# Kernel optimization log

Hardware: AMD Instinct MI355X
Metric: run time of the kernel (lower is better)

The kernel has to match this reference:

```python
import jax, jax.numpy as jnp
import numpy as np
import math

B, S, D, H = 2, 2048, 1024, 16
HD = D // H  # head_dim = 64


def setup_inputs() -> dict:
    rng = jax.random.key(0)
    ks = jax.random.split(rng, 11)
    std = 1.0 / math.sqrt(D)
    inp = {
        "query": jax.random.normal(ks[0], (B, S, D), dtype=jnp.float32),
        "key": jax.random.normal(ks[1], (B, S, D), dtype=jnp.float32),
        "value": jax.random.normal(ks[2], (B, S, D), dtype=jnp.float32),
        # causal mask: True = masked (ignored), matching masked_fill semantics
        "mask": jnp.triu(jnp.ones((S, S), dtype=bool), k=1),
        "wq": jax.random.normal(ks[3], (D, D), dtype=jnp.float32) * std,
        "bq": jnp.zeros((D,), dtype=jnp.float32),
        "wk": jax.random.normal(ks[4], (D, D), dtype=jnp.float32) * std,
        "bk": jnp.zeros((D,), dtype=jnp.float32),
        "wv": jax.random.normal(ks[5], (D, D), dtype=jnp.float32) * std,
        "bv": jnp.zeros((D,), dtype=jnp.float32),
        "wo": jax.random.normal(ks[6], (D, D), dtype=jnp.float32) * std,
        "bo": jnp.zeros((D,), dtype=jnp.float32),
    }
    return inp


def reference(query, key, value, mask, wq, bq, wk, bk, wv, bv, wo, bo):
    # Linear projections (torch Linear: x @ W.T + b)
    q = jnp.einsum('bsd,ed->bse', query, wq) + bq
    k = jnp.einsum('bsd,ed->bse', key, wk) + bk
    v = jnp.einsum('bsd,ed->bse', value, wv) + bv
    # split heads: (B, S, D) -> (B, H, S, HD)
    q = q.reshape(B, S, H, HD).transpose(0, 2, 1, 3)
    k = k.reshape(B, S, H, HD).transpose(0, 2, 1, 3)
    v = v.reshape(B, S, H, HD).transpose(0, 2, 1, 3)
    # naive attention: materialize full (B, H, Sq, Sk) scores
    scores = jnp.einsum('bhqd,bhkd->bhqk', q, k) / jnp.sqrt(jnp.float32(HD))
    scores = jnp.where(mask[None, None, :, :], -jnp.inf, scores)
    attn = jax.nn.softmax(scores, axis=-1)
    out = jnp.einsum('bhqk,bhkd->bhqd', attn, v)
    out = out.transpose(0, 2, 1, 3).reshape(B, S, D)
    return jnp.einsum('bsd,ed->bse', out, wo) + bo
```

## Files before the change

kernel.cpp:

```cpp
#include <hip/hip_runtime.h>
#include <stdint.h>

#define B_ 2
#define S_ 2048
#define D_ 1024
#define H_ 16
#define HD_ 64
#define M_TOT (B_*S_)

typedef __bf16 bf16;
typedef bf16 bf16x8 __attribute__((ext_vector_type(8)));
typedef float f32x4 __attribute__((ext_vector_type(4)));
typedef float f32x16 __attribute__((ext_vector_type(16)));
typedef unsigned int u32;
typedef unsigned int u32x4v __attribute__((ext_vector_type(4)));

__device__ __forceinline__ void gload_lds16(const void* g, void* l) {
    __builtin_amdgcn_global_load_lds((const __attribute__((address_space(1))) void*)g,
                                     (__attribute__((address_space(3))) void*)l, 16, 0, 0);
}

__device__ __forceinline__ u32 cvtpk_bf16(float lo, float hi) {
    u32 d;
    asm("v_cvt_pk_bf16_f32 %0, %1, %2" : "=v"(d) : "v"(lo), "v"(hi));
    return d;
}

__global__ __launch_bounds__(256) void cvt_kernel(
    const float* __restrict__ q, const float* __restrict__ k, const float* __restrict__ v,
    const float* __restrict__ wq, const float* __restrict__ wk,
    const float* __restrict__ wv, const float* __restrict__ wo,
    bf16* __restrict__ xq, bf16* __restrict__ xk, bf16* __restrict__ xv,
    bf16* __restrict__ wqb, bf16* __restrict__ wkb, bf16* __restrict__ wvb, bf16* __restrict__ wob)
{
    const float* src; bf16* dst; int n;
    switch (blockIdx.y) {
        case 0: src=q;  dst=xq;  n=M_TOT*D_; break;
        case 1: src=k;  dst=xk;  n=M_TOT*D_; break;
        case 2: src=v;  dst=xv;  n=M_TOT*D_; break;
        case 3: src=wq; dst=wqb; n=D_*D_;    break;
        case 4: src=wk; dst=wkb; n=D_*D_;    break;
        case 5: src=wv; dst=wvb; n=D_*D_;    break;
        default: src=wo; dst=wob; n=D_*D_;   break;
    }
    int i = (blockIdx.x*blockDim.x + threadIdx.x)*8;
    if (i >= n) return;
    const f32x4* s4 = (const f32x4*)(src + i);
    f32x4 a = s4[0], b = s4[1];
    bf16x8 o;
    #pragma unroll
    for (int j = 0; j < 4; ++j) { o[j] = (bf16)a[j]; o[j+4] = (bf16)b[j]; }
    *(bf16x8*)(dst + i) = o;
}

__device__ __forceinline__ void gemm_mainloop(const bf16* __restrict__ A, const bf16* __restrict__ Wt,
                                              int brow, int bcol, bf16* As, bf16* Bs,
                                              f32x4 (&acc)[4][4])
{
    const int tid = threadIdx.x;
    const int l = tid & 63, w = tid >> 6;
    const int wr = w >> 1, wc = w & 1;
    const int lr = l & 15, lq = l >> 4;

    for (int k0 = 0; k0 < D_; k0 += 32) {
        #pragma unroll
        for (int i = 0; i < 2; ++i) {
            int id = i*256 + tid;
            int row = id >> 2, c8 = (id & 3) << 3;
            gload_lds16(A  + (size_t)(brow + row)*D_ + k0 + c8, As + id*8);
            gload_lds16(Wt + (size_t)(bcol + row)*D_ + k0 + c8, Bs + id*8);
        }
        __syncthreads();
        bf16x8 af[4], bf[4];
        #pragma unroll
        for (int m = 0; m < 4; ++m)
            af[m] = *(const bf16x8*)&As[(wr*64 + m*16 + lr)*32 + lq*8];
        #pragma unroll
        for (int n = 0; n < 4; ++n)
            bf[n] = *(const bf16x8*)&Bs[(wc*64 + n*16 + lr)*32 + lq*8];
        #pragma unroll
        for (int m = 0; m < 4; ++m)
            #pragma unroll
            for (int n = 0; n < 4; ++n)
                acc[m][n] = __builtin_amdgcn_mfma_f32_16x16x32_bf16(af[m], bf[n], acc[m][n], 0, 0, 0);
        __syncthreads();
    }
}

__global__ __launch_bounds__(256) void gemm_qkv(
    const bf16* __restrict__ xq, const bf16* __restrict__ xk, const bf16* __restrict__ xv,
    const bf16* __restrict__ wqb, const bf16* __restrict__ wkb, const bf16* __restrict__ wvb,
    const float* __restrict__ bq, const float* __restrict__ bk, const float* __restrict__ bv,
    bf16* __restrict__ Qf, bf16* __restrict__ Kf, bf16* __restrict__ Vf)
{
    __shared__ __align__(16) bf16 As[128*32];
    __shared__ __align__(16) bf16 Bs[128*32];
    const int z = blockIdx.z;
    const bf16* A  = (z==0) ? xq  : (z==1) ? xk  : xv;
    const bf16* Wt = (z==0) ? wqb : (z==1) ? wkb : wvb;
    const float* bias = (z==0) ? bq : (z==1) ? bk : bv;

    const int brow = (blockIdx.x & 31)*128;
    const int bcol = (blockIdx.x >> 5)*128;

    f32x4 acc[4][4] = {};
    gemm_mainloop(A, Wt, brow, bcol, As, Bs, acc);

    const int tid = threadIdx.x;
    const int l = tid & 63, w = tid >> 6;
    const int wr = w >> 1, wc = w & 1;
    const int lr = l & 15, lq = l >> 4;

    #pragma unroll
    for (int m = 0; m < 4; ++m)
        #pragma unroll
        for (int n = 0; n < 4; ++n) {
            int col = bcol + wc*64 + n*16 + lr;
            float bv_ = bias[col];
            int h = col >> 6, hd = col & 63;
            #pragma unroll
            for (int r = 0; r < 4; ++r) {
                int row = brow + wr*64 + m*16 + lq*4 + r;
                int b = row >> 11, s = row & 2047;
                float val = acc[m][n][r] + bv_;
                if (z == 0) val *= 0.18033688011112042f;
                size_t hbase = ((size_t)b*H_ + h)*S_*HD_;
                if (z < 2) {
                    int chunk = ((s >> 5) << 2) + (hd >> 4);
                    int lane  = (((hd >> 3) & 1) << 5) | (s & 31);
                    bf16* dst = (z==0) ? Qf : Kf;
                    dst[hbase + (size_t)chunk*512 + lane*8 + (hd & 7)] = (bf16)val;
                } else {
                    int chunk = ((s >> 6) << 3) + (((s >> 4) & 3) << 1) + (hd >> 5);
                    int lane  = (((s >> 3) & 1) << 5) | (hd & 31);
                    Vf[hbase + (size_t)chunk*512 + lane*8 + (s & 7)] = (bf16)val;
                }
            }
        }
}

__global__ __launch_bounds__(256) void gemm_out(
    const bf16* __restrict__ Oat, const bf16* __restrict__ wob,
    const float* __restrict__ bo, float* __restrict__ out)
{
    __shared__ __align__(16) bf16 As[128*32];
    __shared__ __align__(16) bf16 Bs[128*32];
    const int brow = (blockIdx.x & 31)*128;
    const int bcol = (blockIdx.x >> 5)*128;

    f32x4 acc[4][4] = {};
    gemm_mainloop(Oat, wob, brow, bcol, As, Bs, acc);

    const int tid = threadIdx.x;
    const int l = tid & 63, w = tid >> 6;
    const int wr = w >> 1, wc = w & 1;
    const int lr = l & 15, lq = l >> 4;

    #pragma unroll
    for (int m = 0; m < 4; ++m)
        #pragma unroll
        for (int n = 0; n < 4; ++n) {
            int col = bcol + wc*64 + n*16 + lr;
            float bv_ = bo[col];
            #pragma unroll
            for (int r = 0; r < 4; ++r) {
                int row = brow + wr*64 + m*16 + lq*4 + r;
                out[(size_t)row*D_ + col] = acc[m][n][r] + bv_;
            }
        }
}

#define ATTN_BODY(CUR, NXT, KT) do {                                                        \
    const int kc0_ = (KT)*64;                                                               \
    const bool last_ = ((KT) == nkt - 1);                                                   \
    const int ktn_ = ((KT) + 1 < nkt) ? (KT) + 1 : (KT);                                    \
    _Pragma("unroll")                                                                       \
    for (int kv2 = 0; kv2 < 2; ++kv2)                                                       \
        _Pragma("unroll")                                                                   \
        for (int dc = 0; dc < 4; ++dc)                                                      \
            NXT[kv2][dc] = *(const bf16x8*)(Kfp + (size_t)((ktn_*2 + kv2)*4 + dc)*512 + l8);\
    bf16x8 va0[4], va1[4];                                                                  \
    _Pragma("unroll")                                                                       \
    for (int c = 0; c < 4; ++c) {                                                           \
        va0[c] = *(const bf16x8*)(Vfp + (size_t)((KT)*8 + c*2 + 0)*512 + l8);               \
        va1[c] = *(const bf16x8*)(Vfp + (size_t)((KT)*8 + c*2 + 1)*512 + l8);               \
    }                                                                                       \
    f32x16 ct0 = {}, ct1 = {};                                                              \
    _Pragma("unroll")                                                                       \
    for (int dc = 0; dc < 4; ++dc)                                                          \
        ct0 = __builtin_amdgcn_mfma_f32_32x32x16_bf16(CUR[0][dc], qb[dc], ct0, 0, 0, 0);    \
    _Pragma("unroll")                                                                       \
    for (int dc = 0; dc < 4; ++dc)                                                          \
        ct1 = __builtin_amdgcn_mfma_f32_32x32x16_bf16(CUR[1][dc], qb[dc], ct1, 0, 0, 0);    \
    if (last_) {                                                                            \
        _Pragma("unroll")                                                                   \
        for (int reg = 0; reg < 16; ++reg) {                                                \
            const int rr = (reg & 3) + 8*(reg >> 2) + 4*hi;                                 \
            if (kc0_ + rr > qrow)      ct0[reg] = -1e30f;                                   \
            if (kc0_ + 32 + rr > qrow) ct1[reg] = -1e30f;                                   \
        }                                                                                   \
    }                                                                                       \
    float t8[8];                                                                            \
    _Pragma("unroll")                                                                       \
    for (int i = 0; i < 8; ++i)                                                             \
        t8[i] = fmaxf(fmaxf(ct0[i], ct0[i+8]), fmaxf(ct1[i], ct1[i+8]));                    \
    float t4a = fmaxf(t8[0], t8[4]), t4b = fmaxf(t8[1], t8[5]);                             \
    float t4c = fmaxf(t8[2], t8[6]), t4d = fmaxf(t8[3], t8[7]);                             \
    float vm = fmaxf(fmaxf(t4a, t4b), fmaxf(t4c, t4d));                                     \
    vm = fmaxf(vm, __shfl_xor(vm, 32));                                                     \
    if (!__all(vm <= mrun + 8.f)) {                                                         \
        float nm = fmaxf(mrun, vm);                                                         \
        float al = exp2f(mrun - nm);                                                        \
        _Pragma("unroll")                                                                   \
        for (int i = 0; i < 16; ++i) { ot0[i] *= al; ot1[i] *= al; }                        \
        lrun *= al;                                                                         \
        mrun = nm;                                                                          \
    }                                                                                       \
    _Pragma("unroll")                                                                       \
    for (int i = 0; i < 16; ++i) {                                                          \
        ct0[i] = exp2f(ct0[i] - mrun);                                                      \
        ct1[i] = exp2f(ct1[i] - mrun);                                                      \
    }                                                                                       \
    float s8[8];                                                                            \
    _Pragma("unroll")                                                                       \
    for (int i = 0; i < 8; ++i)                                                             \
        s8[i] = (ct0[i] + ct0[i+8]) + (ct1[i] + ct1[i+8]);                                  \
    float s4a = s8[0]+s8[4], s4b = s8[1]+s8[5], s4c = s8[2]+s8[6], s4d = s8[3]+s8[7];       \
    float ps = (s4a + s4b) + (s4c + s4d);                                                   \
    ps += __shfl_xor(ps, 32);                                                               \
    lrun += ps;                                                                             \
    u32 own0[8], own1[8], oth0[8], oth1[8];                                                 \
    _Pragma("unroll")                                                                       \
    for (int u = 0; u < 8; ++u) {                                                           \
        own0[u] = cvtpk_bf16(ct0[2*u], ct0[2*u+1]);                                         \
        own1[u] = cvtpk_bf16(ct1[2*u], ct1[2*u+1]);                                         \
    }                                                                                       \
    _Pragma("unroll")                                                                       \
    for (int u = 0; u < 8; ++u) {                                                           \
        oth0[u] = __shfl_xor(own0[u], 32);                                                  \
        oth1[u] = __shfl_xor(own1[u], 32);                                                  \
    }                                                                                       \
    _Pragma("unroll")                                                                       \
    for (int c = 0; c < 4; ++c) {                                                           \
        const int b0 = 4*(c & 1);                                                           \
        u32 o0, o1, o2, o3, x0, x1, x2, x3;                                                 \
        if ((c >> 1) == 0) {                                                                \
            o0 = own0[b0]; o1 = own0[b0+1]; o2 = own0[b0+2]; o3 = own0[b0+3];               \
            x0 = oth0[b0]; x1 = oth0[b0+1]; x2 = oth0[b0+2]; x3 = oth0[b0+3];               \
        } else {                                                                            \
            o0 = own1[b0]; o1 = own1[b0+1]; o2 = own1[b0+2]; o3 = own1[b0+3];               \
            x0 = oth1[b0]; x1 = oth1[b0+1]; x2 = oth1[b0+2]; x3 = oth1[b0+3];               \
        }                                                                                   \
        u32 w0 = hi ? x2 : o0;                                                              \
        u32 w1 = hi ? x3 : o1;                                                              \
        u32 w2 = hi ? o2 : x0;                                                              \
        u32 w3 = hi ? o3 : x1;                                                              \
        u32x4v pw = { w0, w1, w2, w3 };                                                     \
        bf16x8 pb = __builtin_bit_cast(bf16x8, pw);                                         \
        ot0 = __builtin_amdgcn_mfma_f32_32x32x16_bf16(va0[c], pb, ot0, 0, 0, 0);            \
        ot1 = __builtin_amdgcn_mfma_f32_32x32x16_bf16(va1[c], pb, ot1, 0, 0, 0);            \
    }                                                                                       \
} while (0)

__global__ __launch_bounds__(64, 2) void attn_kernel(
    const bf16* __restrict__ Qf, const bf16* __restrict__ Kf,
    const bf16* __restrict__ Vf, bf16* __restrict__ Oat)
{
    __shared__ __align__(16) char Osm[32*128];

    const int l = threadIdx.x & 63;
    const int l31 = l & 31, hi = l >> 5;

    const int id = (int)blockIdx.x;
    const int xcd = id & 7, slot = id >> 3;
    const int bh  = xcd + 8*(slot >> 6);
    const int s6 = slot & 63;
    const int sb = s6 & 31;
    const int g  = ((sb & 7) << 3) | (sb >> 3);
    const int qt = (s6 < 32) ? g : 63 - g;
    const int b = bh >> 4, h = bh & 15;
    const int q0 = qt*32;
    const int qrow = q0 + l31;

    const bf16* Qfp = Qf + (size_t)bh*S_*HD_;
    const bf16* Kfp = Kf + (size_t)bh*S_*HD_;
    const bf16* Vfp = Vf + (size_t)bh*S_*HD_;
    const int l8 = l*8;

    bf16x8 qb[4];
    #pragma unroll
    for (int dc = 0; dc < 4; ++dc)
        qb[dc] = *(const bf16x8*)(Qfp + (size_t)(((q0 >> 5) << 2) + dc)*512 + l8);

    f32x16 ot0 = {}, ot1 = {};
    float mrun = -1e30f, lrun = 0.f;
    const int nkt = q0/64 + 1;

    bf16x8 ka[2][4], kb[2][4];
    #pragma unroll
    for (int kv2 = 0; kv2 < 2; ++kv2)
        #pragma unroll
        for (int dc = 0; dc < 4; ++dc)
            ka[kv2][dc] = *(const bf16x8*)(Kfp + (size_t)(kv2*4 + dc)*512 + l8);

    int kt = 0;
    while (kt + 1 < nkt) {
        ATTN_BODY(ka, kb, kt); ++kt;
        ATTN_BODY(kb, ka, kt); ++kt;
    }
    if (kt < nkt) {
        ATTN_BODY(ka, kb, kt);
    }

    const float inv = 1.f / lrun;
    #pragma unroll
    for (int rp = 0; rp < 16; rp += 2) {
        const int d0 = (rp & 3) + 8*(rp >> 2) + 4*hi;
        u32 p0 = cvtpk_bf16(ot0[rp]*inv, ot0[rp+1]*inv);
        u32 p1 = cvtpk_bf16(ot1[rp]*inv, ot1[rp+1]*inv);
        const int swz = (l31 & 7) << 4;
        *(u32*)(Osm + l31*128 + (( d0*2)        ^ swz)) = p0;
        *(u32*)(Osm + l31*128 + (((32 + d0)*2)  ^ swz)) = p1;
    }
    #pragma unroll
    for (int p = 0; p < 4; ++p) {
        const int row  = p*8 + (l >> 3);
        const int colb = (l & 7)*16;
        u32x4v v = *(const u32x4v*)(Osm + row*128 + (colb ^ ((row & 7) << 4)));
        char* gp = (char*)Oat + (((size_t)(b*S_ + q0 + row)*D_ + h*64)*2) + colb;
        *(u32x4v*)gp = v;
    }
}

extern "C" void kernel_launch(void* const* d_in, const int* in_sizes, int n_in,
                              void* d_out, int out_size, void* d_ws, size_t ws_size,
                              hipStream_t stream) {
    const float* q  = (const float*)d_in[0];
    const float* k  = (const float*)d_in[1];
    const float* v  = (const float*)d_in[2];
    const float* wq = (const float*)d_in[4];
    const float* bq = (const float*)d_in[5];
    const float* wk = (const float*)d_in[6];
    const float* bk = (const float*)d_in[7];
    const float* wv = (const float*)d_in[8];
    const float* bv = (const float*)d_in[9];
    const float* wo = (const float*)d_in[10];
    const float* bo = (const float*)d_in[11];
    float* out = (float*)d_out;

    char* p = (char*)d_ws;
    const size_t XSZ = (size_t)M_TOT*D_*sizeof(bf16);
    const size_t WSZ = (size_t)D_*D_*sizeof(bf16);
    bf16* xq  = (bf16*)p; p += XSZ;
    bf16* xk  = (bf16*)p; p += XSZ;
    bf16* xv  = (bf16*)p; p += XSZ;
    bf16* wqb = (bf16*)p; p += WSZ;
    bf16* wkb = (bf16*)p; p += WSZ;
    bf16* wvb = (bf16*)p; p += WSZ;
    bf16* wob = (bf16*)p; p += WSZ;
    bf16* Qf  = (bf16*)p; p += XSZ;
    bf16* Kf  = (bf16*)p; p += XSZ;
    bf16* Vf  = (bf16*)p; p += XSZ;
    bf16* Oat = (bf16*)p; p += XSZ;

    cvt_kernel<<<dim3(2048, 7), 256, 0, stream>>>(q, k, v, wq, wk, wv, wo,
                                                  xq, xk, xv, wqb, wkb, wvb, wob);
    gemm_qkv<<<dim3(256, 1, 3), 256, 0, stream>>>(xq, xk, xv, wqb, wkb, wvb,
                                                  bq, bk, bv, Qf, Kf, Vf);
    attn_kernel<<<2048, 64, 0, stream>>>(Qf, Kf, Vf, Oat);
    gemm_out<<<dim3(256), 256, 0, stream>>>(Oat, wob, bo, out);
}
```

Baseline: 139.6 us.

## Software-pipeline attention: compute next tile's QK scores during current softmax

```diff
diff --git a/kernel.cpp b/kernel.cpp
--- a/kernel.cpp
+++ b/kernel.cpp
@@ -170,40 +170,46 @@
         }
 }
 
-#define ATTN_BODY(CUR, NXT, KT) do {                                                        \
-    const int kc0_ = (KT)*64;                                                               \
-    const bool last_ = ((KT) == nkt - 1);                                                   \
-    const int ktn_ = ((KT) + 1 < nkt) ? (KT) + 1 : (KT);                                    \
-    _Pragma("unroll")                                                                       \
-    for (int kv2 = 0; kv2 < 2; ++kv2)                                                       \
+#define PIPE_ITER(CT0, CT1, NT0, NT1, KN, KP, T) do {                                       \
+    const int T_ = (T);                                                                     \
+    const int kc0_ = T_*64;                                                                 \
+    const bool last_ = (T_ == nkt - 1);                                                     \
+    if (T_ + 2 < nkt) {                                                                     \
+        _Pragma("unroll")                                                                   \
+        for (int kv2 = 0; kv2 < 2; ++kv2)                                                   \
+            _Pragma("unroll")                                                               \
+            for (int dc = 0; dc < 4; ++dc)                                                  \
+                KP[kv2][dc] = *(const bf16x8*)(Kfp + (size_t)(((T_+2)*2 + kv2)*4 + dc)*512 + l8); \
+    }                                                                                       \
+    bf16x8 va0[4], va1[4];                                                                  \
+    _Pragma("unroll")                                                                       \
+    for (int c = 0; c < 4; ++c) {                                                           \
+        va0[c] = *(const bf16x8*)(Vfp + (size_t)(T_*8 + c*2 + 0)*512 + l8);                 \
+        va1[c] = *(const bf16x8*)(Vfp + (size_t)(T_*8 + c*2 + 1)*512 + l8);                 \
+    }                                                                                       \
+    if (T_ + 1 < nkt) {                                                                     \
+        NT0 = (f32x16){}; NT1 = (f32x16){};                                                 \
+        __builtin_amdgcn_s_setprio(1);                                                      \
         _Pragma("unroll")                                                                   \
         for (int dc = 0; dc < 4; ++dc)                                                      \
-            NXT[kv2][dc] = *(const bf16x8*)(Kfp + (size_t)((ktn_*2 + kv2)*4 + dc)*512 + l8);\
-    bf16x8 va0[4], va1[4];                                                                  \
-    _Pragma("unroll")                                                                       \
-    for (int c = 0; c < 4; ++c) {                                                           \
-        va0[c] = *(const bf16x8*)(Vfp + (size_t)((KT)*8 + c*2 + 0)*512 + l8);               \
-        va1[c] = *(const bf16x8*)(Vfp + (size_t)((KT)*8 + c*2 + 1)*512 + l8);               \
-    }                                                                                       \
-    f32x16 ct0 = {}, ct1 = {};                                                              \
-    _Pragma("unroll")                                                                       \
-    for (int dc = 0; dc < 4; ++dc)                                                          \
-        ct0 = __builtin_amdgcn_mfma_f32_32x32x16_bf16(CUR[0][dc], qb[dc], ct0, 0, 0, 0);    \
-    _Pragma("unroll")                                                                       \
-    for (int dc = 0; dc < 4; ++dc)                                                          \
-        ct1 = __builtin_amdgcn_mfma_f32_32x32x16_bf16(CUR[1][dc], qb[dc], ct1, 0, 0, 0);    \
+            NT0 = __builtin_amdgcn_mfma_f32_32x32x16_bf16(KN[0][dc], qb[dc], NT0, 0, 0, 0); \
+        _Pragma("unroll")                                                                   \
+        for (int dc = 0; dc < 4; ++dc)                                                      \
+            NT1 = __builtin_amdgcn_mfma_f32_32x32x16_bf16(KN[1][dc], qb[dc], NT1, 0, 0, 0); \
+        __builtin_amdgcn_s_setprio(0);                                                      \
+    }                                                                                       \
     if (last_) {                                                                            \
         _Pragma("unroll")                                                                   \
         for (int reg = 0; reg < 16; ++reg) {                                                \
             const int rr = (reg & 3) + 8*(reg >> 2) + 4*hi;                                 \
-            if (kc0_ + rr > qrow)      ct0[reg] = -1e30f;                                   \
-            if (kc0_ + 32 + rr > qrow) ct1[reg] = -1e30f;                                   \
+            if (kc0_ + rr > qrow)      CT0[reg] = -1e30f;                                   \
+            if (kc0_ + 32 + rr > qrow) CT1[reg] = -1e30f;                                   \
         }                                                                                   \
     }                                                                                       \
     float t8[8];                                                                            \
     _Pragma("unroll")                                                                       \
     for (int i = 0; i < 8; ++i)                                                             \
-        t8[i] = fmaxf(fmaxf(ct0[i], ct0[i+8]), fmaxf(ct1[i], ct1[i+8]));                    \
+        t8[i] = fmaxf(fmaxf(CT0[i], CT0[i+8]), fmaxf(CT1[i], CT1[i+8]));                    \
     float t4a = fmaxf(t8[0], t8[4]), t4b = fmaxf(t8[1], t8[5]);                             \
     float t4c = fmaxf(t8[2], t8[6]), t4d = fmaxf(t8[3], t8[7]);                             \
     float vm = fmaxf(fmaxf(t4a, t4b), fmaxf(t4c, t4d));                                     \
@@ -218,48 +224,58 @@
     }                                                                                       \
     _Pragma("unroll")                                                                       \
     for (int i = 0; i < 16; ++i) {                                                          \
-        ct0[i] = exp2f(ct0[i] - mrun);                                                      \
-        ct1[i] = exp2f(ct1[i] - mrun);                                                      \
+        CT0[i] = exp2f(CT0[i] - mrun);                                                      \
+        CT1[i] = exp2f(CT1[i] - mrun);                                                      \
     }                                                                                       \
     float s8[8];                                                                            \
     _Pragma("unroll")                                                                       \
     for (int i = 0; i < 8; ++i)                                                             \
-        s8[i] = (ct0[i] + ct0[i+8]) + (ct1[i] + ct1[i+8]);                                  \
+        s8[i] = (CT0[i] + CT0[i+8]) + (CT1[i] + CT1[i+8]);                                  \
     float s4a = s8[0]+s8[4], s4b = s8[1]+s8[5], s4c = s8[2]+s8[6], s4d = s8[3]+s8[7];       \
     float ps = (s4a + s4b) + (s4c + s4d);                                                   \
     ps += __shfl_xor(ps, 32);                                                               \
     lrun += ps;                                                                             \
-    u32 own0[8], own1[8], oth0[8], oth1[8];                                                 \
+    u32 own0[8], own1[8];                                                                   \
     _Pragma("unroll")                                                                       \
     for (int u = 0; u < 8; ++u) {                                                           \
-        own0[u] = cvtpk_bf16(ct0[2*u], ct0[2*u+1]);                                         \
-        own1[u] = cvtpk_bf16(ct1[2*u], ct1[2*u+1]);                                         \
-    }                                                                                       \
-    _Pragma("unroll")                                                                       \
-    for (int u = 0; u < 8; ++u) {                                                           \
-        oth0[u] = __shfl_xor(own0[u], 32);                                                  \
-        oth1[u] = __shfl_xor(own1[u], 32);                                                  \
-    }                                                                                       \
+        own0[u] = cvtpk_bf16(CT0[2*u], CT0[2*u+1]);                                         \
+        own1[u] = cvtpk_bf16(CT1[2*u], CT1[2*u+1]);                                         \
+    }                                                                                       \
+                   \
+    u32 rcv0[4], rcv1[4];                                                                   \
+    {                                                                                       \
+        u32 s0_ = hi ? own0[0] : own0[2];  u32 s1_ = hi ? own0[1] : own0[3];                \
+        u32 s2_ = hi ? own0[4] : own0[6];  u32 s3_ = hi ? own0[5] : own0[7];                \
+        rcv0[0] = __shfl_xor(s0_, 32); rcv0[1] = __shfl_xor(s1_, 32);                       \
+        rcv0[2] = __shfl_xor(s2_, 32); rcv0[3] = __shfl_xor(s3_, 32);                       \
+        u32 t0_ = hi ? own1[0] : own1[2];  u32 t1_ = hi ? own1[1] : own1[3];                \
+        u32 t2_ = hi ? own1[4] : own1[6];  u32 t3_ = hi ? own1[5] : own1[7];                \
+        rcv1[0] = __shfl_xor(t0_, 32); rcv1[1] = __shfl_xor(t1_, 32);                       \
+        rcv1[2] = __shfl_xor(t2_, 32); rcv1[3] = __shfl_xor(t3_, 32);                       \
+    }                                                                                       \
+    __builtin_amdgcn_s_setprio(1);                                                          \
     _Pragma("unroll")                                                                       \
     for (int c = 0; c < 4; ++c) {                                                           \
         const int b0 = 4*(c & 1);                                                           \
-        u32 o0, o1, o2, o3, x0, x1, x2, x3;                                                 \
+        const int p0 = b0 >> 1;                                                             \
+        u32 oa, ob, oc, od, ra, rb;                                                         \
         if ((c >> 1) == 0) {                                                                \
-            o0 = own0[b0]; o1 = own0[b0+1]; o2 = own0[b0+2]; o3 = own0[b0+3];               \
-            x0 = oth0[b0]; x1 = oth0[b0+1]; x2 = oth0[b0+2]; x3 = oth0[b0+3];               \
+            oa = own0[b0]; ob = own0[b0+1]; oc = own0[b0+2]; od = own0[b0+3];               \
+            ra = rcv0[p0]; rb = rcv0[p0+1];                                                 \
         } else {                                                                            \
-            o0 = own1[b0]; o1 = own1[b0+1]; o2 = own1[b0+2]; o3 = own1[b0+3];               \
-            x0 = oth1[b0]; x1 = oth1[b0+1]; x2 = oth1[b0+2]; x3 = oth1[b0+3];               \
+            oa = own1[b0]; ob = own1[b0+1]; oc = own1[b0+2]; od = own1[b0+3];               \
+            ra = rcv1[p0]; rb = rcv1[p0+1];                                                 \
         }                                                                                   \
-        u32 w0 = hi ? x2 : o0;                                                              \
-        u32 w1 = hi ? x3 : o1;                                                              \
-        u32 w2 = hi ? o2 : x0;                                                              \
-        u32 w3 = hi ? o3 : x1;                                                              \
+        u32 w0 = hi ? ra : oa;                                                              \
+        u32 w1 = hi ? rb : ob;                                                              \
+        u32 w2 = hi ? oc : ra;                                                              \
+        u32 w3 = hi ? od : rb;                                                              \
         u32x4v pw = { w0, w1, w2, w3 };                                                     \
         bf16x8 pb = __builtin_bit_cast(bf16x8, pw);                                         \
         ot0 = __builtin_amdgcn_mfma_f32_32x32x16_bf16(va0[c], pb, ot0, 0, 0, 0);            \
         ot1 = __builtin_amdgcn_mfma_f32_32x32x16_bf16(va1[c], pb, ot1, 0, 0, 0);            \
     }                                                                                       \
+    __builtin_amdgcn_s_setprio(0);                                                          \
 } while (0)
 
 __global__ __launch_bounds__(64, 2) void attn_kernel(
@@ -270,6 +286,7 @@
 
     const int l = threadIdx.x & 63;
     const int l31 = l & 31, hi = l >> 5;
+    const int l8 = l*8;
 
     const int id = (int)blockIdx.x;
     const int xcd = id & 7, slot = id >> 3;
@@ -285,7 +302,6 @@
     const bf16* Qfp = Qf + (size_t)bh*S_*HD_;
     const bf16* Kfp = Kf + (size_t)bh*S_*HD_;
     const bf16* Vfp = Vf + (size_t)bh*S_*HD_;
-    const int l8 = l*8;
 
     bf16x8 qb[4];
     #pragma unroll
@@ -302,14 +318,26 @@
         #pragma unroll
         for (int dc = 0; dc < 4; ++dc)
             ka[kv2][dc] = *(const bf16x8*)(Kfp + (size_t)(kv2*4 + dc)*512 + l8);
-
-    int kt = 0;
-    while (kt + 1 < nkt) {
-        ATTN_BODY(ka, kb, kt); ++kt;
-        ATTN_BODY(kb, ka, kt); ++kt;
-    }
-    if (kt < nkt) {
-        ATTN_BODY(ka, kb, kt);
+    #pragma unroll
+    for (int kv2 = 0; kv2 < 2; ++kv2)
+        #pragma unroll
+        for (int dc = 0; dc < 4; ++dc)
+            kb[kv2][dc] = *(const bf16x8*)(Kfp + (size_t)((2 + kv2)*4 + dc)*512 + l8);
+
+    f32x16 ctA0 = {}, ctA1 = {}, ctB0 = {}, ctB1 = {};
+    #pragma unroll
+    for (int dc = 0; dc < 4; ++dc)
+        ctA0 = __builtin_amdgcn_mfma_f32_32x32x16_bf16(ka[0][dc], qb[dc], ctA0, 0, 0, 0);
+    #pragma unroll
+    for (int dc = 0; dc < 4; ++dc)
+        ctA1 = __builtin_amdgcn_mfma_f32_32x32x16_bf16(ka[1][dc], qb[dc], ctA1, 0, 0, 0);
+
+    int t = 0;
+    for (;;) {
+        PIPE_ITER(ctA0, ctA1, ctB0, ctB1, kb, ka, t);
+        if (++t >= nkt) break;
+        PIPE_ITER(ctB0, ctB1, ctA0, ctA1, ka, kb, t);
+        if (++t >= nkt) break;
     }
 
     const float inv = 1.f / lrun;
```

Measured after the change: 141.5 us. About the same (+1.3%).

## Split attention KV range across two workgroups and merge with combine kernel

Applied to the files above, without the earlier changes.

```diff
diff --git a/kernel.cpp b/kernel.cpp
--- a/kernel.cpp
+++ b/kernel.cpp
@@ -173,7 +173,7 @@
 #define ATTN_BODY(CUR, NXT, KT) do {                                                        \
     const int kc0_ = (KT)*64;                                                               \
     const bool last_ = ((KT) == nkt - 1);                                                   \
-    const int ktn_ = ((KT) + 1 < nkt) ? (KT) + 1 : (KT);                                    \
+    const int ktn_ = ((KT) + 1 < te) ? (KT) + 1 : (KT);                                     \
     _Pragma("unroll")                                                                       \
     for (int kv2 = 0; kv2 < 2; ++kv2)                                                       \
         _Pragma("unroll")                                                                   \
@@ -186,12 +186,14 @@
         va1[c] = *(const bf16x8*)(Vfp + (size_t)((KT)*8 + c*2 + 1)*512 + l8);               \
     }                                                                                       \
     f32x16 ct0 = {}, ct1 = {};                                                              \
+    __builtin_amdgcn_s_setprio(1);                                                          \
     _Pragma("unroll")                                                                       \
     for (int dc = 0; dc < 4; ++dc)                                                          \
         ct0 = __builtin_amdgcn_mfma_f32_32x32x16_bf16(CUR[0][dc], qb[dc], ct0, 0, 0, 0);    \
     _Pragma("unroll")                                                                       \
     for (int dc = 0; dc < 4; ++dc)                                                          \
         ct1 = __builtin_amdgcn_mfma_f32_32x32x16_bf16(CUR[1][dc], qb[dc], ct1, 0, 0, 0);    \
+    __builtin_amdgcn_s_setprio(0);                                                          \
     if (last_) {                                                                            \
         _Pragma("unroll")                                                                   \
         for (int reg = 0; reg < 16; ++reg) {                                                \
@@ -240,6 +242,7 @@
         oth0[u] = __shfl_xor(own0[u], 32);                                                  \
         oth1[u] = __shfl_xor(own1[u], 32);                                                  \
     }                                                                                       \
+    __builtin_amdgcn_s_setprio(1);                                                          \
     _Pragma("unroll")                                                                       \
     for (int c = 0; c < 4; ++c) {                                                           \
         const int b0 = 4*(c & 1);                                                           \
@@ -260,32 +263,34 @@
         ot0 = __builtin_amdgcn_mfma_f32_32x32x16_bf16(va0[c], pb, ot0, 0, 0, 0);            \
         ot1 = __builtin_amdgcn_mfma_f32_32x32x16_bf16(va1[c], pb, ot1, 0, 0, 0);            \
     }                                                                                       \
+    __builtin_amdgcn_s_setprio(0);                                                          \
 } while (0)
 
-__global__ __launch_bounds__(64, 2) void attn_kernel(
+__global__ __launch_bounds__(64, 4) void attn_part(
     const bf16* __restrict__ Qf, const bf16* __restrict__ Kf,
-    const bf16* __restrict__ Vf, bf16* __restrict__ Oat)
-{
-    __shared__ __align__(16) char Osm[32*128];
-
+    const bf16* __restrict__ Vf, bf16* __restrict__ Opart, float* __restrict__ Mlf)
+{
     const int l = threadIdx.x & 63;
     const int l31 = l & 31, hi = l >> 5;
+    const int l8 = l*8;
 
     const int id = (int)blockIdx.x;
-    const int xcd = id & 7, slot = id >> 3;
-    const int bh  = xcd + 8*(slot >> 6);
-    const int s6 = slot & 63;
-    const int sb = s6 & 31;
-    const int g  = ((sb & 7) << 3) | (sb >> 3);
-    const int qt = (s6 < 32) ? g : 63 - g;
-    const int b = bh >> 4, h = bh & 15;
+    const int bh = id >> 7;
+    const int rem = id & 127;
+    const int qt = 63 - (rem >> 1);
+    const int half = rem & 1;
     const int q0 = qt*32;
     const int qrow = q0 + l31;
+    const int widx = (bh*64 + qt)*2 + half;
 
     const bf16* Qfp = Qf + (size_t)bh*S_*HD_;
     const bf16* Kfp = Kf + (size_t)bh*S_*HD_;
     const bf16* Vfp = Vf + (size_t)bh*S_*HD_;
-    const int l8 = l*8;
+
+    const int nkt = q0/64 + 1;
+    const int nh0 = nkt - (nkt >> 1);
+    const int ts = half ? nh0 : 0;
+    const int te = half ? nkt : nh0;
 
     bf16x8 qb[4];
     #pragma unroll
@@ -294,41 +299,66 @@
 
     f32x16 ot0 = {}, ot1 = {};
     float mrun = -1e30f, lrun = 0.f;
-    const int nkt = q0/64 + 1;
-
-    bf16x8 ka[2][4], kb[2][4];
-    #pragma unroll
-    for (int kv2 = 0; kv2 < 2; ++kv2)
-        #pragma unroll
-        for (int dc = 0; dc < 4; ++dc)
-            ka[kv2][dc] = *(const bf16x8*)(Kfp + (size_t)(kv2*4 + dc)*512 + l8);
-
-    int kt = 0;
-    while (kt + 1 < nkt) {
-        ATTN_BODY(ka, kb, kt); ++kt;
-        ATTN_BODY(kb, ka, kt); ++kt;
-    }
-    if (kt < nkt) {
-        ATTN_BODY(ka, kb, kt);
-    }
-
-    const float inv = 1.f / lrun;
-    #pragma unroll
-    for (int rp = 0; rp < 16; rp += 2) {
+
+    if (ts < te) {
+        bf16x8 ka[2][4], kb[2][4];
+        #pragma unroll
+        for (int kv2 = 0; kv2 < 2; ++kv2)
+            #pragma unroll
+            for (int dc = 0; dc < 4; ++dc)
+                ka[kv2][dc] = *(const bf16x8*)(Kfp + (size_t)((ts*2 + kv2)*4 + dc)*512 + l8);
+
+        int kt = ts;
+        while (kt + 1 < te) {
+            ATTN_BODY(ka, kb, kt); ++kt;
+            ATTN_BODY(kb, ka, kt); ++kt;
+        }
+        if (kt < te) {
+            ATTN_BODY(ka, kb, kt);
+        }
+    }
+
+    bf16* Ob = Opart + (size_t)widx*2048;
+    #pragma unroll
+    for (int rp = 0; rp < 16; ++rp) {
         const int d0 = (rp & 3) + 8*(rp >> 2) + 4*hi;
-        u32 p0 = cvtpk_bf16(ot0[rp]*inv, ot0[rp+1]*inv);
-        u32 p1 = cvtpk_bf16(ot1[rp]*inv, ot1[rp+1]*inv);
-        const int swz = (l31 & 7) << 4;
-        *(u32*)(Osm + l31*128 + (( d0*2)        ^ swz)) = p0;
-        *(u32*)(Osm + l31*128 + (((32 + d0)*2)  ^ swz)) = p1;
-    }
-    #pragma unroll
-    for (int p = 0; p < 4; ++p) {
-        const int row  = p*8 + (l >> 3);
-        const int colb = (l & 7)*16;
-        u32x4v v = *(const u32x4v*)(Osm + row*128 + (colb ^ ((row & 7) << 4)));
-        char* gp = (char*)Oat + (((size_t)(b*S_ + q0 + row)*D_ + h*64)*2) + colb;
-        *(u32x4v*)gp = v;
+        Ob[d0*32 + l31]        = (bf16)ot0[rp];
+        Ob[(32 + d0)*32 + l31] = (bf16)ot1[rp];
+    }
+    if (!hi) {
+        Mlf[(size_t)widx*64 + l31*2]     = mrun;
+        Mlf[(size_t)widx*64 + l31*2 + 1] = lrun;
+    }
+}
+
+__global__ __launch_bounds__(64) void attn_combine(
+    const bf16* __restrict__ Opart, const float* __restrict__ Mlf, bf16* __restrict__ Oat)
+{
+    const int cb = (int)blockIdx.x;
+    const int bh = cb >> 6, qt = cb & 63;
+    const int b = bh >> 4, h = bh & 15;
+    const int q0 = qt*32;
+    const int l = threadIdx.x & 63;
+    const int q = l & 31, hi = l >> 5;
+
+    const int w0 = (bh*64 + qt)*2, w1 = w0 + 1;
+    const float m0 = Mlf[(size_t)w0*64 + q*2],     l0 = Mlf[(size_t)w0*64 + q*2 + 1];
+    const float m1 = Mlf[(size_t)w1*64 + q*2],     l1 = Mlf[(size_t)w1*64 + q*2 + 1];
+    const float m = fmaxf(m0, m1);
+    const float a0 = exp2f(m0 - m), a1 = exp2f(m1 - m);
+    const float inv = 1.f / (l0*a0 + l1*a1);
+    const float f0 = a0*inv, f1 = a1*inv;
+
+    const bf16* O0 = Opart + (size_t)w0*2048;
+    const bf16* O1 = Opart + (size_t)w1*2048;
+    char* rowp = (char*)Oat + (((size_t)(b*S_ + q0 + q)*D_ + h*64 + hi*32)*2);
+
+    #pragma unroll
+    for (int i = 0; i < 16; ++i) {
+        const int d = hi*32 + 2*i;
+        float oA = (float)O0[d*32 + q]*f0       + (float)O1[d*32 + q]*f1;
+        float oB = (float)O0[(d+1)*32 + q]*f0   + (float)O1[(d+1)*32 + q]*f1;
+        *(u32*)(rowp + 4*i) = cvtpk_bf16(oA, oB);
     }
 }
 
@@ -351,22 +381,25 @@
     char* p = (char*)d_ws;
     const size_t XSZ = (size_t)M_TOT*D_*sizeof(bf16);
     const size_t WSZ = (size_t)D_*D_*sizeof(bf16);
-    bf16* xq  = (bf16*)p; p += XSZ;
-    bf16* xk  = (bf16*)p; p += XSZ;
-    bf16* xv  = (bf16*)p; p += XSZ;
-    bf16* wqb = (bf16*)p; p += WSZ;
-    bf16* wkb = (bf16*)p; p += WSZ;
-    bf16* wvb = (bf16*)p; p += WSZ;
-    bf16* wob = (bf16*)p; p += WSZ;
-    bf16* Qf  = (bf16*)p; p += XSZ;
-    bf16* Kf  = (bf16*)p; p += XSZ;
-    bf16* Vf  = (bf16*)p; p += XSZ;
-    bf16* Oat = (bf16*)p; p += XSZ;
+    bf16* xq  = (bf16*)p;
+    bf16* xk  = (bf16*)(p + XSZ);
+    bf16* xv  = (bf16*)(p + 2*XSZ);
+    bf16* wqb = (bf16*)(p + 3*XSZ);
+    bf16* wkb = (bf16*)(p + 3*XSZ + WSZ);
+    bf16* wvb = (bf16*)(p + 3*XSZ + 2*WSZ);
+    bf16* wob = (bf16*)(p + 3*XSZ + 3*WSZ);
+    bf16* Qf  = (bf16*)(p + 3*XSZ + 4*WSZ);
+    bf16* Kf  = Qf + M_TOT*D_;
+    bf16* Vf  = Kf + M_TOT*D_;
+    bf16* Oat = Vf + M_TOT*D_;
+    bf16*  Opart = (bf16*)p;
+    float* Mlf   = (float*)(p + 2*XSZ);
 
     cvt_kernel<<<dim3(2048, 7), 256, 0, stream>>>(q, k, v, wq, wk, wv, wo,
                                                   xq, xk, xv, wqb, wkb, wvb, wob);
     gemm_qkv<<<dim3(256, 1, 3), 256, 0, stream>>>(xq, xk, xv, wqb, wkb, wvb,
                                                   bq, bk, bv, Qf, Kf, Vf);
-    attn_kernel<<<2048, 64, 0, stream>>>(Qf, Kf, Vf, Oat);
+    attn_part<<<4096, 64, 0, stream>>>(Qf, Kf, Vf, Opart, Mlf);
+    attn_combine<<<2048, 64, 0, stream>>>(Opart, Mlf, Oat);
     gemm_out<<<dim3(256), 256, 0, stream>>>(Oat, wob, bo, out);
 }
```

New measurement: 293.5 us. +110.2%, slower.
